# Kernel optimization log

Measured on AMD Instinct MI355X. Metric: run time of the kernel, lower is better.

Reference implementation:

```python
import jax, jax.numpy as jnp
import numpy as np

NUM_BEV_FEATURES = 64
NX, NY, NZ = 432, 496, 1
G = NZ * NX * NY  # flattened BEV grid size per sample
B, P = 4, 12000   # batch size, pillars per sample


def setup_inputs() -> dict:
    key = jax.random.key(0)
    kf, kc = jax.random.split(key)
    pillar_features = jax.random.normal(kf, (B, NUM_BEV_FEATURES, P, 1), dtype=jnp.float32)
    # Unique spatial indices per batch sample (avoids duplicate-scatter ambiguity)
    perm = jax.vmap(lambda k: jax.random.permutation(k, G)[:P])(jax.random.split(kc, B))  # [B, P]
    bidx = jnp.repeat(jnp.arange(B), P)  # matches view(-1, C) flattening order
    coords = jnp.stack([bidx, perm.reshape(-1)], axis=1).astype(jnp.int64)  # [B*P, 2]
    return {"pillar_features": pillar_features, "coords": coords}


def reference(pillar_features, coords):
    b, c, p, _ = pillar_features.shape
    # [B, C, P, 1] -> [B*P, C] (same flattening as permute(0,2,1).view(-1,C))
    feats = pillar_features[..., 0].transpose(0, 2, 1).reshape(b * p, c)
    batch_idx = coords[:, 0]
    spatial_idx = coords[:, 1]
    mask = spatial_idx > 0  # module drops pillars with spatial index 0
    # Fused scatter: global index = batch*G + spatial; masked rows -> OOB -> dropped
    idx = jnp.where(mask, batch_idx * G + spatial_idx, b * G)
    out = jnp.zeros((b * G, c), dtype=feats.dtype).at[idx].set(feats, mode="drop")
    # [B*G, C] -> [B, C, G] -> [B, C*nz, ny, nx]
    return out.reshape(b, G, c).transpose(0, 2, 1).reshape(b, c * NZ, NY, NX)
```

## Files before the change

kernel.cpp:

```cpp
#include <hip/hip_runtime.h>


namespace {
constexpr int kB = 4;
constexpr int kP = 12000;
constexpr int kC = 64;
constexpr int kG = 432 * 496;
constexpr int kGq = kG / 4;
constexpr int kCSplit = 8;
constexpr int kCPer = kC / kCSplit;
}

__global__ __launch_bounds__(256) void build_inv_kernel(const int* __restrict__ coords,
                                                        int* __restrict__ inv) {
    int i = blockIdx.x * blockDim.x + threadIdx.x;
    if (i >= kB * kP) return;
    int b = coords[2 * i];
    int s = coords[2 * i + 1];
    if (s > 0 && s < kG && b >= 0 && b < kB) inv[b * kG + s] = i;
}

__global__ __launch_bounds__(256) void bev_gather_kernel(const float* __restrict__ pf,
                                                         const int* __restrict__ inv,
                                                         float* __restrict__ out) {
    int t = blockIdx.x * blockDim.x + threadIdx.x;
    int gq = t % kGq;
    int bc = t / kGq;
    int cc = bc & (kCSplit - 1);
    int b = bc >> 3;
    if (b >= kB) return;

    const int4 iv = *reinterpret_cast<const int4*>(inv + b * kG + 4 * gq);

    float a0[kCPer], a1[kCPer], a2[kCPer], a3[kCPer];
#pragma unroll
    for (int j = 0; j < kCPer; ++j) {
        a0[j] = 0.f; a1[j] = 0.f; a2[j] = 0.f; a3[j] = 0.f;
    }

    const int c0 = cc * kCPer;

    if (iv.x >= 0) {
        const float* src = pf + (iv.x / kP) * (kC * kP) + (iv.x % kP) + c0 * kP;
#pragma unroll
        for (int j = 0; j < kCPer; ++j) a0[j] = src[j * kP];
    }
    if (iv.y >= 0) {
        const float* src = pf + (iv.y / kP) * (kC * kP) + (iv.y % kP) + c0 * kP;
#pragma unroll
        for (int j = 0; j < kCPer; ++j) a1[j] = src[j * kP];
    }
    if (iv.z >= 0) {
        const float* src = pf + (iv.z / kP) * (kC * kP) + (iv.z % kP) + c0 * kP;
#pragma unroll
        for (int j = 0; j < kCPer; ++j) a2[j] = src[j * kP];
    }
    if (iv.w >= 0) {
        const float* src = pf + (iv.w / kP) * (kC * kP) + (iv.w % kP) + c0 * kP;
#pragma unroll
        for (int j = 0; j < kCPer; ++j) a3[j] = src[j * kP];
    }

    float* ob = out + (size_t)b * kC * kG + (size_t)c0 * kG + 4 * gq;
#pragma unroll
    for (int j = 0; j < kCPer; ++j) {
        float4 v = make_float4(a0[j], a1[j], a2[j], a3[j]);
        *reinterpret_cast<float4*>(ob + (size_t)j * kG) = v;
    }
}

extern "C" void kernel_launch(void* const* d_in, const int* in_sizes, int n_in,
                              void* d_out, int out_size, void* d_ws, size_t ws_size,
                              hipStream_t stream) {
    const float* pf = (const float*)d_in[0];
    const int* coords = (const int*)d_in[1];
    float* out = (float*)d_out;
    int* inv = (int*)d_ws;

    hipMemsetAsync(inv, 0xFF, (size_t)kB * kG * sizeof(int), stream);

    build_inv_kernel<<<(kB * kP + 255) / 256, 256, 0, stream>>>(coords, inv);

    const int total = kB * kCSplit * kGq;
    bev_gather_kernel<<<total / 256, 256, 0, stream>>>(pf, inv, out);
}
```

Before: 243.9 us.

## Pre-transpose pillar features to row-major for vectorized gather, use nontemporal stores

Adds a shared-memory transpose kernel that turns the [B,C,P] pillar features into [B*P,C], so the gather kernel reads each pillar's 8-channel slice as two 16-byte vector loads instead of eight strided scalar loads. Output stores to the large BEV grid become nontemporal stores to limit cache pollution. The cost is an extra kernel launch plus roughly 12 MB of workspace traffic for the transposed copy.

Result: faster. 236.6 us (-3.0%).

```diff
diff --git a/kernel.cpp b/kernel.cpp
--- a/kernel.cpp
+++ b/kernel.cpp
@@ -9,6 +9,8 @@
 constexpr int kGq = kG / 4;
 constexpr int kCSplit = 8;
 constexpr int kCPer = kC / kCSplit;
+constexpr int kTP = 64;
+typedef float floatx4 __attribute__((ext_vector_type(4)));
 }
 
 __global__ __launch_bounds__(256) void build_inv_kernel(const int* __restrict__ coords,
@@ -20,7 +22,39 @@
     if (s > 0 && s < kG && b >= 0 && b < kB) inv[b * kG + s] = i;
 }
 
-__global__ __launch_bounds__(256) void bev_gather_kernel(const float* __restrict__ pf,
+__global__ __launch_bounds__(256) void transpose_kernel(const float* __restrict__ pf,
+                                                        float* __restrict__ ft) {
+    __shared__ float tile[kC][kTP + 1];
+    const int b = blockIdx.y;
+    const int p0 = blockIdx.x * kTP;
+    const int tx = threadIdx.x % kTP;
+    const int tg = threadIdx.x / kTP;
+    const int p = p0 + tx;
+
+    if (p < kP) {
+#pragma unroll
+        for (int it = 0; it < 16; ++it) {
+            int c = it * 4 + tg;
+            tile[c][tx] = pf[((size_t)b * kC + c) * kP + p];
+        }
+    }
+    __syncthreads();
+
+    const int q = threadIdx.x % 16;
+    const int r = threadIdx.x / 16;
+#pragma unroll
+    for (int rr = 0; rr < 4; ++rr) {
+        int pp = rr * 16 + r;
+        int prow = p0 + pp;
+        if (prow < kP) {
+            floatx4 v = {tile[4 * q + 0][pp], tile[4 * q + 1][pp],
+                         tile[4 * q + 2][pp], tile[4 * q + 3][pp]};
+            *reinterpret_cast<floatx4*>(ft + ((size_t)b * kP + prow) * kC + 4 * q) = v;
+        }
+    }
+}
+
+__global__ __launch_bounds__(256) void bev_gather_kernel(const float* __restrict__ ft,
                                                          const int* __restrict__ inv,
                                                          float* __restrict__ out) {
     int t = blockIdx.x * blockDim.x + threadIdx.x;
@@ -31,41 +65,38 @@
     if (b >= kB) return;
 
     const int4 iv = *reinterpret_cast<const int4*>(inv + b * kG + 4 * gq);
+    const int c0 = cc * kCPer;
 
     float a0[kCPer], a1[kCPer], a2[kCPer], a3[kCPer];
 #pragma unroll
-    for (int j = 0; j < kCPer; ++j) {
-        a0[j] = 0.f; a1[j] = 0.f; a2[j] = 0.f; a3[j] = 0.f;
-    }
-
-    const int c0 = cc * kCPer;
+    for (int j = 0; j < kCPer; ++j) { a0[j] = 0.f; a1[j] = 0.f; a2[j] = 0.f; a3[j] = 0.f; }
 
     if (iv.x >= 0) {
-        const float* src = pf + (iv.x / kP) * (kC * kP) + (iv.x % kP) + c0 * kP;
-#pragma unroll
-        for (int j = 0; j < kCPer; ++j) a0[j] = src[j * kP];
+        const floatx4* s = reinterpret_cast<const floatx4*>(ft + (size_t)iv.x * kC + c0);
+        *reinterpret_cast<floatx4*>(&a0[0]) = s[0];
+        *reinterpret_cast<floatx4*>(&a0[4]) = s[1];
     }
     if (iv.y >= 0) {
-        const float* src = pf + (iv.y / kP) * (kC * kP) + (iv.y % kP) + c0 * kP;
-#pragma unroll
-        for (int j = 0; j < kCPer; ++j) a1[j] = src[j * kP];
+        const floatx4* s = reinterpret_cast<const floatx4*>(ft + (size_t)iv.y * kC + c0);
+        *reinterpret_cast<floatx4*>(&a1[0]) = s[0];
+        *reinterpret_cast<floatx4*>(&a1[4]) = s[1];
     }
     if (iv.z >= 0) {
-        const float* src = pf + (iv.z / kP) * (kC * kP) + (iv.z % kP) + c0 * kP;
-#pragma unroll
-        for (int j = 0; j < kCPer; ++j) a2[j] = src[j * kP];
+        const floatx4* s = reinterpret_cast<const floatx4*>(ft + (size_t)iv.z * kC + c0);
+        *reinterpret_cast<floatx4*>(&a2[0]) = s[0];
+        *reinterpret_cast<floatx4*>(&a2[4]) = s[1];
     }
     if (iv.w >= 0) {
-        const float* src = pf + (iv.w / kP) * (kC * kP) + (iv.w % kP) + c0 * kP;
-#pragma unroll
-        for (int j = 0; j < kCPer; ++j) a3[j] = src[j * kP];
+        const floatx4* s = reinterpret_cast<const floatx4*>(ft + (size_t)iv.w * kC + c0);
+        *reinterpret_cast<floatx4*>(&a3[0]) = s[0];
+        *reinterpret_cast<floatx4*>(&a3[4]) = s[1];
     }
 
     float* ob = out + (size_t)b * kC * kG + (size_t)c0 * kG + 4 * gq;
 #pragma unroll
     for (int j = 0; j < kCPer; ++j) {
-        float4 v = make_float4(a0[j], a1[j], a2[j], a3[j]);
-        *reinterpret_cast<float4*>(ob + (size_t)j * kG) = v;
+        floatx4 v = {a0[j], a1[j], a2[j], a3[j]};
+        __builtin_nontemporal_store(v, reinterpret_cast<floatx4*>(ob + (size_t)j * kG));
     }
 }
 
@@ -76,11 +107,15 @@
     const int* coords = (const int*)d_in[1];
     float* out = (float*)d_out;
     int* inv = (int*)d_ws;
+    float* ft = (float*)((char*)d_ws + (size_t)kB * kG * sizeof(int));
 
-    hipMemsetAsync(inv, 0xFF, (size_t)kB * kG * sizeof(int), stream);
+    (void)hipMemsetAsync(inv, 0xFF, (size_t)kB * kG * sizeof(int), stream);
 
     build_inv_kernel<<<(kB * kP + 255) / 256, 256, 0, stream>>>(coords, inv);
 
+    dim3 tgrid((kP + kTP - 1) / kTP, kB);
+    transpose_kernel<<<tgrid, 256, 0, stream>>>(pf, ft);
+
     const int total = kB * kCSplit * kGq;
-    bev_gather_kernel<<<total / 256, 256, 0, stream>>>(pf, inv, out);
+    bev_gather_kernel<<<total / 256, 256, 0, stream>>>(ft, inv, out);
 }
```
